# Performance work log

Hardware: AMD Instinct MI355X
Metric: run time of the kernel (lower is better)

The kernel has to match this reference:

```python
import jax, jax.numpy as jnp
import numpy as np

B, T, C, H, HS = 4, 2048, 1024, 16, 64
EPS = 1e-5


def setup_inputs() -> dict:
    key = jax.random.key(0)
    ks = jax.random.split(key, 16)
    s = lambda k, shp, fan: jax.random.normal(k, shp, jnp.float32) * (fan ** -0.5)
    return {
        "x": jax.random.normal(ks[0], (B, T, C), jnp.float32),
        "wq": s(ks[1], (H, C, HS), C), "bq": jnp.zeros((H, HS), jnp.float32),
        "wk": s(ks[2], (H, C, HS), C), "bk": jnp.zeros((H, HS), jnp.float32),
        "wv": s(ks[3], (H, C, HS), C), "bv": jnp.zeros((H, HS), jnp.float32),
        "wp": s(ks[4], (C, C), C), "bp": jnp.zeros((C,), jnp.float32),
        "w1": s(ks[5], (C, 4 * C), C), "b1": jnp.zeros((4 * C,), jnp.float32),
        "w2": s(ks[6], (4 * C, C), 4 * C), "b2": jnp.zeros((C,), jnp.float32),
        "g1": jnp.ones((C,), jnp.float32), "be1": jnp.zeros((C,), jnp.float32),
        "g2": jnp.ones((C,), jnp.float32), "be2": jnp.zeros((C,), jnp.float32),
    }


def _layernorm(x, g, b):
    mu = jnp.mean(x, axis=-1, keepdims=True)
    var = jnp.mean(jnp.square(x - mu), axis=-1, keepdims=True)
    return (x - mu) * jax.lax.rsqrt(var + EPS) * g + b


def reference(x, wq, bq, wk, bk, wv, bv, wp, bp, w1, b1, w2, b2, g1, be1, g2, be2):
    Bc, Tc, Cc = x.shape
    h = _layernorm(x, g1, be1)
    # per-head projections stacked: [B,H,T,HS]
    q = jnp.einsum('btc,hcd->bhtd', h, wq) + bq[None, :, None, :]
    k = jnp.einsum('btc,hcd->bhtd', h, wk) + bk[None, :, None, :]
    v = jnp.einsum('btc,hcd->bhtd', h, wv) + bv[None, :, None, :]
    # NOTE: source scales by 1/sqrt(n_embd), not 1/sqrt(head_size)
    scores = jnp.einsum('bhtd,bhsd->bhts', q, k) * (Cc ** -0.5)
    causal = jnp.tril(jnp.ones((Tc, Tc), bool))
    scores = jnp.where(causal, scores, -jnp.inf)
    attn = jax.nn.softmax(scores, axis=-1)
    out = jnp.einsum('bhts,bhsd->bhtd', attn, v)
    out = out.transpose(0, 2, 1, 3).reshape(Bc, Tc, Cc)  # concat heads
    x = x + out @ wp + bp
    h2 = _layernorm(x, g2, be2)
    ffn = jax.nn.relu(h2 @ w1 + b1) @ w2 + b2
    return x + ffn
```

## Files before the change

kernel.cpp:

```cpp
#include <hip/hip_runtime.h>


constexpr int Bb = 4, Tt = 2048, Cc = 1024, Hh = 16, HSz = 64, Ff = 4096;
constexpr int Mrows = Bb * Tt;

typedef __attribute__((ext_vector_type(8))) short bf16x8;
typedef __attribute__((ext_vector_type(4))) float f32x4;

__device__ __forceinline__ ushort f2bf(float f) {
  uint u = __builtin_bit_cast(uint, f);
  uint r = (u + 0x7fffu + ((u >> 16) & 1u)) >> 16;
  return (ushort)r;
}
__device__ __forceinline__ float bf2f(ushort s) {
  return __builtin_bit_cast(float, ((uint)s) << 16);
}
__device__ __forceinline__ uint cvtpk_bf16(float lo, float hi) {
  uint r;
  asm("v_cvt_pk_bf16_f32 %0, %1, %2" : "=v"(r) : "v"(lo), "v"(hi));
  return r;
}
__device__ __forceinline__ void gload16(const void* g, void* l) {
  __builtin_amdgcn_global_load_lds(
      (const __attribute__((address_space(1))) void*)g,
      (__attribute__((address_space(3))) void*)l, 16, 0, 0);
}
#define VMCNT0 asm volatile("s_waitcnt vmcnt(0)" ::: "memory")
#define LGKM0                                        \
  do {                                               \
    asm volatile("s_waitcnt lgkmcnt(0)" ::: "memory"); \
    __builtin_amdgcn_sched_barrier(0);               \
  } while (0)
#define BARRIER __builtin_amdgcn_s_barrier()

__global__ __launch_bounds__(256) void ln_kernel(const float* __restrict__ x,
                                                 const float* __restrict__ g,
                                                 const float* __restrict__ b,
                                                 ushort* __restrict__ out) {
  int row = blockIdx.x;
  const float* xr = x + (size_t)row * Cc;
  int c4 = threadIdx.x * 4;
  float4 v = *(const float4*)(xr + c4);
  float s1 = v.x + v.y + v.z + v.w;
  float s2 = v.x * v.x + v.y * v.y + v.z * v.z + v.w * v.w;
#pragma unroll
  for (int off = 32; off >= 1; off >>= 1) {
    s1 += __shfl_xor(s1, off);
    s2 += __shfl_xor(s2, off);
  }
  __shared__ float red[8];
  int wid = threadIdx.x >> 6, lane = threadIdx.x & 63;
  if (lane == 0) { red[wid] = s1; red[4 + wid] = s2; }
  __syncthreads();
  float t1 = red[0] + red[1] + red[2] + red[3];
  float t2 = red[4] + red[5] + red[6] + red[7];
  float mu = t1 * (1.0f / Cc);
  float var = t2 * (1.0f / Cc) - mu * mu;
  float rs = rsqrtf(var + 1e-5f);
  float4 gv = *(const float4*)(g + c4);
  float4 bv = *(const float4*)(b + c4);
  ushort4 o;
  o.x = f2bf((v.x - mu) * rs * gv.x + bv.x);
  o.y = f2bf((v.y - mu) * rs * gv.y + bv.y);
  o.z = f2bf((v.z - mu) * rs * gv.z + bv.z);
  o.w = f2bf((v.w - mu) * rs * gv.w + bv.w);
  *(ushort4*)(out + (size_t)row * Cc + c4) = o;
}

__device__ __forceinline__ void tcast_body(const float* __restrict__ src,
                                           ushort* __restrict__ dst, int ldS,
                                           int ldD, int r0, int c0) {
  __shared__ float t[32][33];
  int c = threadIdx.x & 31, r8 = threadIdx.x >> 5;
#pragma unroll
  for (int i = 0; i < 4; ++i) {
    int r = r8 + i * 8;
    t[r][c] = src[(size_t)(r0 + r) * ldS + c0 + c];
  }
  __syncthreads();
#pragma unroll
  for (int i = 0; i < 4; ++i) {
    int rr = r8 + i * 8;
    dst[(size_t)(c0 + rr) * ldD + r0 + c] = f2bf(t[c][rr]);
  }
}

__global__ __launch_bounds__(256) void tcast_kernel(const float* __restrict__ src,
                                                    ushort* __restrict__ dst,
                                                    int ldS, int ldD) {
  tcast_body(src, dst, ldS, ldD, blockIdx.x * 32, blockIdx.y * 32);
}

__global__ __launch_bounds__(256) void tcast_qkv(const float* __restrict__ wq,
                                                 const float* __restrict__ wk,
                                                 const float* __restrict__ wv,
                                                 ushort* __restrict__ dst) {
  int z = blockIdx.z, zz = z >> 4, h = z & 15;
  const float* src = (zz == 0 ? wq : (zz == 1 ? wk : wv)) + (size_t)h * Cc * HSz;
  ushort* d = dst + (size_t)(zz * 1024 + h * 64) * 1024;
  tcast_body(src, d, HSz, Cc, blockIdx.x * 32, blockIdx.y * 32);
}

__global__ __launch_bounds__(256) void bias_concat(const float* __restrict__ bq,
                                                   const float* __restrict__ bk,
                                                   const float* __restrict__ bv,
                                                   float* __restrict__ dst) {
  int i = blockIdx.x * 256 + threadIdx.x;
  dst[i] = i < 1024 ? bq[i] : (i < 2048 ? bk[i - 1024] : bv[i - 2048]);
}

__device__ __forceinline__ void xcd_swz(int& bx, int& by) {
  int bid = blockIdx.x + blockIdx.y * gridDim.x;
  int cpx = (gridDim.x * gridDim.y) >> 3;
  int id = (bid & 7) * cpx + (bid >> 3);
  bx = id % gridDim.x;
  by = id / gridDim.x;
}

template <int MH, int NH>
__device__ __forceinline__ void mfma16(f32x4 (&acc)[8][4], bf16x8 (&a)[4][2],
                                       bf16x8 (&b)[2][2]) {
#pragma unroll
  for (int m = 0; m < 4; ++m)
#pragma unroll
    for (int n = 0; n < 2; ++n)
#pragma unroll
      for (int kk = 0; kk < 2; ++kk)
        acc[MH * 4 + m][NH * 2 + n] = __builtin_amdgcn_mfma_f32_16x16x32_bf16(
            a[m][kk], b[n][kk], acc[MH * 4 + m][NH * 2 + n], 0, 0, 0);
}

__device__ __forceinline__ void gemm256_main(const ushort* __restrict__ A,
                                             const ushort* __restrict__ Bt,
                                             int m0, int n0,
                                             ushort* __restrict__ As,
                                             ushort* __restrict__ Bs,
                                             f32x4 (&acc)[8][4]) {
  constexpr int NKT = 16;
  int tid = threadIdx.x, wid = tid >> 6, lane = tid & 63;
  int wr = wid >> 2, wc = wid & 3, fr = lane & 15, fq = lane >> 4;
  const ushort* Ag = A + (size_t)m0 * 1024;
  const ushort* Bg = Bt + (size_t)n0 * 1024;
  int r0 = tid >> 3, r1 = 64 + (tid >> 3);
  int sc = ((tid & 7) ^ ((tid >> 3) & 7)) << 3;

  auto stage = [&](int ktn, int h, int ns) {
    const ushort* g = (h < 2) ? Ag : Bg;
    ushort* l = ((h < 2) ? As : Bs) + ns * 16384 + (h & 1) * 8192;
    int kcol = ktn * 64, rbase = (h & 1) * 128;
    gload16(g + (size_t)(rbase + r0) * 1024 + kcol + sc, l + (size_t)wid * 512);
    gload16(g + (size_t)(rbase + r1) * 1024 + kcol + sc,
            l + (size_t)(512 + wid * 64) * 8);
  };
  auto readA = [&](int slot, int mh, bf16x8 (&a)[4][2]) {
#pragma unroll
    for (int m = 0; m < 4; ++m) {
      int row = wr * 128 + mh * 64 + m * 16 + fr;
#pragma unroll
      for (int kk = 0; kk < 2; ++kk)
        a[m][kk] = *(const bf16x8*)&As[slot * 16384 + row * 64 +
                                       (((kk * 4 + fq) ^ (row & 7)) << 3)];
    }
  };
  auto readB = [&](int slot, int nh, bf16x8 (&b)[2][2]) {
#pragma unroll
    for (int n = 0; n < 2; ++n) {
      int row = wc * 64 + nh * 32 + n * 16 + fr;
#pragma unroll
      for (int kk = 0; kk < 2; ++kk)
        b[n][kk] = *(const bf16x8*)&Bs[slot * 16384 + row * 64 +
                                       (((kk * 4 + fq) ^ (row & 7)) << 3)];
    }
  };

  stage(0, 0, 0); stage(0, 1, 0); stage(0, 2, 0); stage(0, 3, 0);
  VMCNT0;
  BARRIER;

  bf16x8 a[4][2], b0[2][2], b1[2][2];
#pragma unroll 1
  for (int kt = 0; kt < NKT; ++kt) {
    int slot = kt & 1, ns = slot ^ 1;
    bool st = (kt + 1 < NKT);
    readA(slot, 0, a);
    readB(slot, 0, b0);
    if (st) { stage(kt + 1, 0, ns); stage(kt + 1, 2, ns); }
    BARRIER;
    LGKM0;
    __builtin_amdgcn_s_setprio(1);
    mfma16<0, 0>(acc, a, b0);
    __builtin_amdgcn_s_setprio(0);
    BARRIER;
    readB(slot, 1, b1);
    if (st) { stage(kt + 1, 1, ns); stage(kt + 1, 3, ns); }
    BARRIER;
    LGKM0;
    __builtin_amdgcn_s_setprio(1);
    mfma16<0, 1>(acc, a, b1);
    __builtin_amdgcn_s_setprio(0);
    BARRIER;
    readA(slot, 1, a);
    BARRIER;
    LGKM0;
    __builtin_amdgcn_s_setprio(1);
    mfma16<1, 0>(acc, a, b0);
    __builtin_amdgcn_s_setprio(0);
    BARRIER;
    __builtin_amdgcn_s_setprio(1);
    mfma16<1, 1>(acc, a, b1);
    __builtin_amdgcn_s_setprio(0);
    VMCNT0;
    BARRIER;
  }
}

__global__ __launch_bounds__(512, 2) void gemm256_relu(
    const ushort* __restrict__ A, const ushort* __restrict__ Bt,
    const float* __restrict__ bias, ushort* __restrict__ Cout, int ldc) {
  __shared__ __align__(16) ushort As[2 * 256 * 64];
  __shared__ __align__(16) ushort Bs[2 * 256 * 64];
  f32x4 acc[8][4] = {};
  int bx, by;
  xcd_swz(bx, by);
  int m0 = by * 256, n0 = bx * 256;
  gemm256_main(A, Bt, m0, n0, As, Bs, acc);
  int lane = threadIdx.x & 63, wid = threadIdx.x >> 6;
  int wr = wid >> 2, wc = wid & 3, fr = lane & 15, fq = lane >> 4;
#pragma unroll
  for (int i = 0; i < 8; ++i) {
    int gm = m0 + wr * 128 + (i >> 2) * 64 + (i & 3) * 16 + fq * 4;
#pragma unroll
    for (int j2 = 0; j2 < 4; ++j2) {
      int gn = n0 + wc * 64 + (j2 >> 1) * 32 + (j2 & 1) * 16 + fr;
      float bsv = bias[gn];
#pragma unroll
      for (int j = 0; j < 4; ++j)
        Cout[(size_t)(gm + j) * ldc + gn] = f2bf(fmaxf(acc[i][j2][j] + bsv, 0.f));
    }
  }
}

__global__ __launch_bounds__(512, 2) void gemm256_qkv(
    const ushort* __restrict__ A, const ushort* __restrict__ Bt,
    const float* __restrict__ bias, ushort* __restrict__ q,
    ushort* __restrict__ k, ushort* __restrict__ vt) {
  __shared__ __align__(16) ushort As[2 * 256 * 64];
  __shared__ __align__(16) ushort Bs[2 * 256 * 64];
  f32x4 acc[8][4] = {};
  int bx, by;
  xcd_swz(bx, by);
  int m0 = by * 256, n0 = bx * 256;
  gemm256_main(A, Bt, m0, n0, As, Bs, acc);
  int lane = threadIdx.x & 63, wid = threadIdx.x >> 6;
  int wr = wid >> 2, wc = wid & 3, fr = lane & 15, fq = lane >> 4;
  const float qscale = 1.4426950408889634f / 32.0f;
#pragma unroll
  for (int i = 0; i < 8; ++i) {
    int gm = m0 + wr * 128 + (i >> 2) * 64 + (i & 3) * 16 + fq * 4;
#pragma unroll
    for (int j2 = 0; j2 < 4; ++j2) {
      int gn = n0 + wc * 64 + (j2 >> 1) * 32 + (j2 & 1) * 16 + fr;
      float bsv = bias[gn];
      if (gn < 1024) {
#pragma unroll
        for (int j = 0; j < 4; ++j)
          q[(size_t)(gm + j) * 1024 + gn] = f2bf((acc[i][j2][j] + bsv) * qscale);
      } else if (gn < 2048) {
        int col = gn - 1024;
#pragma unroll
        for (int j = 0; j < 4; ++j)
          k[(size_t)(gm + j) * 1024 + col] = f2bf(acc[i][j2][j] + bsv);
      } else {
        int dd = gn - 2048, h = dd >> 6, d = dd & 63;
        int bbr = gm >> 11, t = gm & 2047;
        ushort4 pw = {f2bf(acc[i][j2][0] + bsv), f2bf(acc[i][j2][1] + bsv),
                      f2bf(acc[i][j2][2] + bsv), f2bf(acc[i][j2][3] + bsv)};
        *(ushort4*)&vt[(((size_t)(bbr * 16 + h)) * 64 + d) * 2048 + t] = pw;
      }
    }
  }
}

__device__ __forceinline__ void gemm_main(const ushort* __restrict__ A, int lda,
                                          const ushort* __restrict__ Bt, int ldb,
                                          int K, int m0, int n0,
                                          ushort* __restrict__ As,
                                          ushort* __restrict__ Bs,
                                          f32x4 (&acc)[4][2]) {
  int tid = threadIdx.x, wid = tid >> 6, lane = tid & 63;
  int wr = wid >> 2, wc = wid & 3, fr = lane & 15, fq = lane >> 4;
  const ushort* Ag = A + (size_t)m0 * lda;
  const ushort* Bg = Bt + (size_t)n0 * ldb;
  for (int k0 = 0; k0 < K; k0 += 64) {
#pragma unroll
    for (int c = 0; c < 2; ++c) {
      int slot = c * 512 + tid;
      int row = slot >> 3, s = slot & 7;
      int sw = (s << 3) ^ ((row & 7) << 3);
      gload16(Ag + (size_t)row * lda + k0 + sw, As + (size_t)(c * 512 + wid * 64) * 8);
      gload16(Bg + (size_t)row * ldb + k0 + sw, Bs + (size_t)(c * 512 + wid * 64) * 8);
    }
    __syncthreads();
    bf16x8 av[4][2], bv[2][2];
#pragma unroll
    for (int m = 0; m < 4; ++m) {
      int row = wr * 64 + m * 16 + fr;
#pragma unroll
      for (int ks = 0; ks < 2; ++ks)
        av[m][ks] = *(const bf16x8*)&As[row * 64 + (((ks * 4 + fq) ^ (row & 7)) << 3)];
    }
#pragma unroll
    for (int n = 0; n < 2; ++n) {
      int row = wc * 32 + n * 16 + fr;
#pragma unroll
      for (int ks = 0; ks < 2; ++ks)
        bv[n][ks] = *(const bf16x8*)&Bs[row * 64 + (((ks * 4 + fq) ^ (row & 7)) << 3)];
    }
#pragma unroll
    for (int m = 0; m < 4; ++m)
#pragma unroll
      for (int n = 0; n < 2; ++n)
#pragma unroll
        for (int ks = 0; ks < 2; ++ks)
          acc[m][n] = __builtin_amdgcn_mfma_f32_16x16x32_bf16(
              av[m][ks], bv[n][ks], acc[m][n], 0, 0, 0);
    __syncthreads();
  }
}

template <bool RELU, bool HASRES, bool OUTBF16>
__global__ __launch_bounds__(512) void gemm_bf16(
    const ushort* __restrict__ A, int lda, const ushort* __restrict__ Bt,
    int ldb, const float* __restrict__ bias, const float* __restrict__ res,
    void* __restrict__ Cout, int ldc, int K) {
  __shared__ __align__(16) ushort As[128 * 64];
  __shared__ __align__(16) ushort Bs[128 * 64];
  f32x4 acc[4][2] = {};
  int bx, by;
  xcd_swz(bx, by);
  int m0 = by * 128, n0 = bx * 128;
  gemm_main(A, lda, Bt, ldb, K, m0, n0, As, Bs, acc);
  int lane = threadIdx.x & 63, wid = threadIdx.x >> 6;
  int wr = wid >> 2, wc = wid & 3, fr = lane & 15, fq = lane >> 4;
#pragma unroll
  for (int m = 0; m < 4; ++m) {
    int gm = m0 + wr * 64 + m * 16 + fq * 4;
#pragma unroll
    for (int n = 0; n < 2; ++n) {
      int gn = n0 + wc * 32 + n * 16 + fr;
      float bsv = bias[gn];
#pragma unroll
      for (int j = 0; j < 4; ++j) {
        int row = gm + j;
        float v = acc[m][n][j] + bsv;
        if constexpr (HASRES) v += res[(size_t)row * ldc + gn];
        if constexpr (RELU) v = fmaxf(v, 0.f);
        if constexpr (OUTBF16)
          ((ushort*)Cout)[(size_t)row * ldc + gn] = f2bf(v);
        else
          ((float*)Cout)[(size_t)row * ldc + gn] = v;
      }
    }
  }
}

constexpr int QB = 128, KVB = 64;
__global__ __launch_bounds__(512) void attn_kernel(const ushort* __restrict__ Qb,
                                                   const ushort* __restrict__ Kb,
                                                   const ushort* __restrict__ Vt,
                                                   ushort* __restrict__ att) {
  __shared__ __align__(16) ushort Klds[2][64 * 64];
  __shared__ __align__(16) ushort Vlds[2][64 * 64];
  __shared__ __align__(16) ushort Plds[8][16 * 64];
  int tid = threadIdx.x, wid = tid >> 6, lane = tid & 63;
  int fr = lane & 15, fq = lane >> 4;
  int bh = blockIdx.y, bb = bh >> 4, hh = bh & 15;
  const ushort* qkbase = Qb + ((size_t)bb * Tt) * Cc + hh * HSz;
  const ushort* Kbase = Kb + ((size_t)bb * Tt) * Cc + hh * HSz;
  const ushort* Vbase = Vt + ((size_t)(bb * Hh + hh)) * HSz * Tt;
  int srow = tid >> 3;
  int ssw = ((tid & 7) << 3) ^ ((srow & 7) << 3);

#pragma unroll 1
  for (int pass = 0; pass < 2; ++pass) {
    int qt = pass ? (Tt / QB - 1 - (int)blockIdx.x) : (int)blockIdx.x;
    int q0 = qt * QB;
    int q0w = q0 + wid * 16;

    bf16x8 Qreg[2];
#pragma unroll
    for (int d2 = 0; d2 < 2; ++d2)
      Qreg[d2] = *(const bf16x8*)(qkbase + (size_t)(q0w + fr) * Cc + d2 * 32 + fq * 8);
    f32x4 Oa[4] = {};
    float mrow = -1e30f, lrow = 0.f;
    int nt = q0 / KVB + 2;

    __syncthreads();
    gload16(Kbase + (size_t)srow * Cc + ssw, (char*)Klds[0] + wid * 1024);
    gload16(Vbase + (size_t)srow * Tt + ssw, (char*)Vlds[0] + wid * 1024);

#pragma unroll 1
    for (int kt = 0; kt < nt; ++kt) {
      int t0 = kt * KVB;
      int c = kt & 1;
      __syncthreads();
      if (kt + 1 < nt) {
        int t0n = t0 + KVB;
        gload16(Kbase + (size_t)(t0n + srow) * Cc + ssw,
                (char*)Klds[c ^ 1] + wid * 1024);
        gload16(Vbase + (size_t)srow * Tt + t0n + ssw,
                (char*)Vlds[c ^ 1] + wid * 1024);
      }
      if (q0w + 15 < t0) continue;

      const char* Kc = (const char*)Klds[c];
      const char* Vc = (const char*)Vlds[c];
      bf16x8 kf[4][2];
#pragma unroll
      for (int ks = 0; ks < 4; ++ks)
#pragma unroll
        for (int d2 = 0; d2 < 2; ++d2) {
          int row = ks * 16 + fr;
          int off = (d2 * 64 + fq * 16) ^ ((row & 7) << 4);
          kf[ks][d2] = *(const bf16x8*)(Kc + row * 128 + off);
        }
      f32x4 accs[4] = {};
      __builtin_amdgcn_s_setprio(1);
#pragma unroll
      for (int ks = 0; ks < 4; ++ks) {
        accs[ks] = __builtin_amdgcn_mfma_f32_16x16x32_bf16(
            kf[ks][0], Qreg[0], accs[ks], 0, 0, 0);
        accs[ks] = __builtin_amdgcn_mfma_f32_16x16x32_bf16(
            kf[ks][1], Qreg[1], accs[ks], 0, 0, 0);
      }
      __builtin_amdgcn_s_setprio(0);

      float sv[4][4];
      float vmax = -1e30f;
      if (t0 + 63 <= q0w) {
#pragma unroll
        for (int ks = 0; ks < 4; ++ks)
#pragma unroll
          for (int j = 0; j < 4; ++j) {
            sv[ks][j] = accs[ks][j];
            vmax = fmaxf(vmax, sv[ks][j]);
          }
      } else {
        int qg = q0w + fr;
#pragma unroll
        for (int ks = 0; ks < 4; ++ks)
#pragma unroll
          for (int j = 0; j < 4; ++j) {
            int kg = t0 + ks * 16 + fq * 4 + j;
            float s = accs[ks][j];
            s = (kg <= qg) ? s : -1e30f;
            sv[ks][j] = s;
            vmax = fmaxf(vmax, s);
          }
      }
      float mnew = mrow;
      if (!__all(vmax <= mrow + 11.0f)) {
        float rmax = fmaxf(vmax, __shfl_xor(vmax, 16));
        rmax = fmaxf(rmax, __shfl_xor(rmax, 32));
        mnew = fmaxf(mrow, rmax);
        float sf = exp2f(mrow - mnew);
        mrow = mnew;
        lrow *= sf;
#pragma unroll
        for (int j = 0; j < 4; ++j) {
          float sfo = __shfl(sf, fq * 4 + j);
#pragma unroll
          for (int ds = 0; ds < 4; ++ds) Oa[ds][j] *= sfo;
        }
      }
      char* pbase = (char*)Plds[wid] + fr * 128;
#pragma unroll
      for (int ks = 0; ks < 4; ++ks) {
        float p0 = exp2f(sv[ks][0] - mnew);
        float p1 = exp2f(sv[ks][1] - mnew);
        float p2 = exp2f(sv[ks][2] - mnew);
        float p3 = exp2f(sv[ks][3] - mnew);
        lrow += (p0 + p1) + (p2 + p3);
        uint2 pw = {cvtpk_bf16(p0, p1), cvtpk_bf16(p2, p3)};
        int off = (ks * 32 + fq * 8) ^ ((fr & 7) << 4);
        *(uint2*)(pbase + off) = pw;
      }

      bf16x8 vf[4][2];
#pragma unroll
      for (int ds = 0; ds < 4; ++ds)
#pragma unroll
        for (int k2 = 0; k2 < 2; ++k2) {
          int row = ds * 16 + fr;
          int off = (k2 * 64 + fq * 16) ^ ((row & 7) << 4);
          vf[ds][k2] = *(const bf16x8*)(Vc + row * 128 + off);
        }
      bf16x8 pf[2];
#pragma unroll
      for (int k2 = 0; k2 < 2; ++k2) {
        int off = (k2 * 64 + fq * 16) ^ ((fr & 7) << 4);
        pf[k2] = *(const bf16x8*)((const char*)Plds[wid] + fr * 128 + off);
      }
      __builtin_amdgcn_s_setprio(1);
#pragma unroll
      for (int ds = 0; ds < 4; ++ds) {
        Oa[ds] = __builtin_amdgcn_mfma_f32_16x16x32_bf16(
            pf[0], vf[ds][0], Oa[ds], 0, 0, 0);
        Oa[ds] = __builtin_amdgcn_mfma_f32_16x16x32_bf16(
            pf[1], vf[ds][1], Oa[ds], 0, 0, 0);
      }
      __builtin_amdgcn_s_setprio(0);
    }

    {
      lrow += __shfl_xor(lrow, 16);
      lrow += __shfl_xor(lrow, 32);
      float linv = 1.f / lrow;
#pragma unroll
      for (int j = 0; j < 4; ++j) {
        float lo = __shfl(linv, fq * 4 + j);
        int qg = q0w + fq * 4 + j;
        ushort* orow = att + (size_t)(bb * Tt + qg) * Cc + hh * HSz;
#pragma unroll
        for (int ds = 0; ds < 4; ++ds)
          orow[ds * 16 + fr] = f2bf(Oa[ds][j] * lo);
      }
    }
  }
}

extern "C" void kernel_launch(void* const* d_in, const int* in_sizes, int n_in,
                              void* d_out, int out_size, void* d_ws,
                              size_t ws_size, hipStream_t stream) {
  const float* x = (const float*)d_in[0];
  const float* wq = (const float*)d_in[1];
  const float* bq = (const float*)d_in[2];
  const float* wk = (const float*)d_in[3];
  const float* bk = (const float*)d_in[4];
  const float* wv = (const float*)d_in[5];
  const float* bv = (const float*)d_in[6];
  const float* wp = (const float*)d_in[7];
  const float* bp = (const float*)d_in[8];
  const float* w1 = (const float*)d_in[9];
  const float* b1 = (const float*)d_in[10];
  const float* w2 = (const float*)d_in[11];
  const float* b2 = (const float*)d_in[12];
  const float* g1 = (const float*)d_in[13];
  const float* be1 = (const float*)d_in[14];
  const float* g2 = (const float*)d_in[15];
  const float* be2 = (const float*)d_in[16];
  float* out = (float*)d_out;

  ushort* Qb = (ushort*)d_ws;
  ushort* Kb = Qb + (size_t)8388608;
  ushort* Vt = Kb + (size_t)8388608;
  ushort* att = Vt + (size_t)8388608;
  ushort* ffh = Qb;
  ushort* h1b = att + (size_t)8388608;
  float* x2 = (float*)(h1b + (size_t)8388608);
  ushort* wqkvT = (ushort*)(x2 + (size_t)8388608);
  ushort* wpT = wqkvT + (size_t)3145728;
  ushort* w1T = wpT + (size_t)1048576;
  ushort* w2T = w1T + (size_t)4194304;
  float* bqkv = (float*)(w2T + (size_t)4194304);

  tcast_qkv<<<dim3(32, 2, 48), 256, 0, stream>>>(wq, wk, wv, wqkvT);
  tcast_kernel<<<dim3(32, 32), 256, 0, stream>>>(wp, wpT, 1024, 1024);
  tcast_kernel<<<dim3(32, 128), 256, 0, stream>>>(w1, w1T, 4096, 1024);
  tcast_kernel<<<dim3(128, 32), 256, 0, stream>>>(w2, w2T, 1024, 4096);
  bias_concat<<<dim3(12), 256, 0, stream>>>(bq, bk, bv, bqkv);

  ln_kernel<<<dim3(Mrows), 256, 0, stream>>>(x, g1, be1, h1b);
  gemm256_qkv<<<dim3(12, 32), 512, 0, stream>>>(h1b, wqkvT, bqkv, Qb, Kb, Vt);
  attn_kernel<<<dim3(Tt / QB / 2, Bb * Hh), 512, 0, stream>>>(Qb, Kb, Vt, att);
  gemm_bf16<false, true, false><<<dim3(8, 64), 512, 0, stream>>>(
      att, 1024, wpT, 1024, bp, x, x2, 1024, 1024);
  ln_kernel<<<dim3(Mrows), 256, 0, stream>>>(x2, g2, be2, h1b);
  gemm256_relu<<<dim3(16, 32), 512, 0, stream>>>(h1b, w1T, b1, ffh, 4096);
  gemm_bf16<false, true, false><<<dim3(8, 64), 512, 0, stream>>>(
      ffh, 4096, w2T, 4096, b2, x2, out, 1024, 4096);
}
```

Baseline: 358.2 us.

## Use 256x128 pipelined GEMM for FFN2 and 128x128 tiles for QKV

Adds a new 256x128-tile FFN down-projection kernel with double-buffered LDS staging, swizzled reads, split MFMA phases and raised wave priority. It replaces the 128x128 generic GEMM for the K=4096 projection and reuses more data per tile. In exchange, the QKV projection moves from the 256x256 kernel to the generic 128x128 kernel, which gives more blocks (1536 vs 384) for better occupancy and balance but less reuse per block. The new FFN2 grid has only 256 blocks, which may underfill the GPU.

```diff
diff --git a/kernel.cpp b/kernel.cpp
--- a/kernel.cpp
+++ b/kernel.cpp
@@ -26,10 +26,10 @@
       (__attribute__((address_space(3))) void*)l, 16, 0, 0);
 }
 #define VMCNT0 asm volatile("s_waitcnt vmcnt(0)" ::: "memory")
-#define LGKM0                                        \
-  do {                                               \
+#define LGKM0                                          \
+  do {                                                 \
     asm volatile("s_waitcnt lgkmcnt(0)" ::: "memory"); \
-    __builtin_amdgcn_sched_barrier(0);               \
+    __builtin_amdgcn_sched_barrier(0);                 \
   } while (0)
 #define BARRIER __builtin_amdgcn_s_barrier()
 
@@ -240,42 +240,114 @@
   }
 }
 
-__global__ __launch_bounds__(512, 2) void gemm256_qkv(
-    const ushort* __restrict__ A, const ushort* __restrict__ Bt,
-    const float* __restrict__ bias, ushort* __restrict__ q,
-    ushort* __restrict__ k, ushort* __restrict__ vt) {
+__global__ __launch_bounds__(512, 2) void gemm256_ffn2(
+    const ushort* __restrict__ A, int lda, const ushort* __restrict__ Bt,
+    int ldb, const float* __restrict__ bias, const float* __restrict__ res,
+    float* __restrict__ Cout, int ldc, int K) {
   __shared__ __align__(16) ushort As[2 * 256 * 64];
-  __shared__ __align__(16) ushort Bs[2 * 256 * 64];
-  f32x4 acc[8][4] = {};
+  __shared__ __align__(16) ushort Bs[2 * 128 * 64];
+  f32x4 acc[8][2] = {};
   int bx, by;
   xcd_swz(bx, by);
-  int m0 = by * 256, n0 = bx * 256;
-  gemm256_main(A, Bt, m0, n0, As, Bs, acc);
-  int lane = threadIdx.x & 63, wid = threadIdx.x >> 6;
+  int m0 = by * 256, n0 = bx * 128;
+  int tid = threadIdx.x, wid = tid >> 6, lane = tid & 63;
   int wr = wid >> 2, wc = wid & 3, fr = lane & 15, fq = lane >> 4;
-  const float qscale = 1.4426950408889634f / 32.0f;
+  const ushort* Ag = A + (size_t)m0 * lda;
+  const ushort* Bg = Bt + (size_t)n0 * ldb;
+  int r0 = tid >> 3, r1 = 64 + (tid >> 3);
+  int sc = ((tid & 7) ^ ((tid >> 3) & 7)) << 3;
+  int NKT = K >> 6;
+
+  auto stageA = [&](int ktn, int h, int ns) {
+    ushort* l = As + ns * 16384 + h * 8192;
+    int kcol = ktn * 64, rbase = h * 128;
+    gload16(Ag + (size_t)(rbase + r0) * lda + kcol + sc, l + (size_t)wid * 512);
+    gload16(Ag + (size_t)(rbase + r1) * lda + kcol + sc,
+            l + (size_t)(512 + wid * 64) * 8);
+  };
+  auto stageB = [&](int ktn, int h, int ns) {
+    ushort* l = Bs + ns * 8192 + h * 4096;
+    int kcol = ktn * 64, rbase = h * 64;
+    gload16(Bg + (size_t)(rbase + r0) * ldb + kcol + sc, l + (size_t)wid * 512);
+  };
+  auto readA = [&](int slot, int mh, bf16x8 (&a)[4][2]) {
+#pragma unroll
+    for (int m = 0; m < 4; ++m) {
+      int row = wr * 128 + mh * 64 + m * 16 + fr;
+#pragma unroll
+      for (int kk = 0; kk < 2; ++kk)
+        a[m][kk] = *(const bf16x8*)&As[slot * 16384 + row * 64 +
+                                       (((kk * 4 + fq) ^ (row & 7)) << 3)];
+    }
+  };
+  auto readB = [&](int slot, int nh, bf16x8 (&b)[2]) {
+    int row = wc * 32 + nh * 16 + fr;
+#pragma unroll
+    for (int kk = 0; kk < 2; ++kk)
+      b[kk] = *(const bf16x8*)&Bs[slot * 8192 + row * 64 +
+                                  (((kk * 4 + fq) ^ (row & 7)) << 3)];
+  };
+  auto mfma8 = [&](int mh, int nh, bf16x8 (&a)[4][2], bf16x8 (&b)[2]) {
+#pragma unroll
+    for (int m = 0; m < 4; ++m)
+#pragma unroll
+      for (int kk = 0; kk < 2; ++kk)
+        acc[mh * 4 + m][nh] = __builtin_amdgcn_mfma_f32_16x16x32_bf16(
+            a[m][kk], b[kk], acc[mh * 4 + m][nh], 0, 0, 0);
+  };
+
+  stageA(0, 0, 0); stageA(0, 1, 0); stageB(0, 0, 0); stageB(0, 1, 0);
+  VMCNT0;
+  BARRIER;
+
+  bf16x8 a[4][2], b0[2], b1[2];
+#pragma unroll 1
+  for (int kt = 0; kt < NKT; ++kt) {
+    int slot = kt & 1, ns = slot ^ 1;
+    bool st = (kt + 1 < NKT);
+    readA(slot, 0, a);
+    readB(slot, 0, b0);
+    if (st) { stageA(kt + 1, 0, ns); stageB(kt + 1, 0, ns); }
+    BARRIER;
+    LGKM0;
+    __builtin_amdgcn_s_setprio(1);
+    mfma8(0, 0, a, b0);
+    __builtin_amdgcn_s_setprio(0);
+    BARRIER;
+    readB(slot, 1, b1);
+    if (st) { stageA(kt + 1, 1, ns); stageB(kt + 1, 1, ns); }
+    BARRIER;
+    LGKM0;
+    __builtin_amdgcn_s_setprio(1);
+    mfma8(0, 1, a, b1);
+    __builtin_amdgcn_s_setprio(0);
+    BARRIER;
+    readA(slot, 1, a);
+    BARRIER;
+    LGKM0;
+    __builtin_amdgcn_s_setprio(1);
+    mfma8(1, 0, a, b0);
+    __builtin_amdgcn_s_setprio(0);
+    BARRIER;
+    __builtin_amdgcn_s_setprio(1);
+    mfma8(1, 1, a, b1);
+    __builtin_amdgcn_s_setprio(0);
+    VMCNT0;
+    BARRIER;
+  }
+
 #pragma unroll
   for (int i = 0; i < 8; ++i) {
     int gm = m0 + wr * 128 + (i >> 2) * 64 + (i & 3) * 16 + fq * 4;
 #pragma unroll
-    for (int j2 = 0; j2 < 4; ++j2) {
-      int gn = n0 + wc * 64 + (j2 >> 1) * 32 + (j2 & 1) * 16 + fr;
+    for (int nh = 0; nh < 2; ++nh) {
+      int gn = n0 + wc * 32 + nh * 16 + fr;
       float bsv = bias[gn];
-      if (gn < 1024) {
-#pragma unroll
-        for (int j = 0; j < 4; ++j)
-          q[(size_t)(gm + j) * 1024 + gn] = f2bf((acc[i][j2][j] + bsv) * qscale);
-      } else if (gn < 2048) {
-        int col = gn - 1024;
-#pragma unroll
-        for (int j = 0; j < 4; ++j)
-          k[(size_t)(gm + j) * 1024 + col] = f2bf(acc[i][j2][j] + bsv);
-      } else {
-        int dd = gn - 2048, h = dd >> 6, d = dd & 63;
-        int bbr = gm >> 11, t = gm & 2047;
-        ushort4 pw = {f2bf(acc[i][j2][0] + bsv), f2bf(acc[i][j2][1] + bsv),
-                      f2bf(acc[i][j2][2] + bsv), f2bf(acc[i][j2][3] + bsv)};
-        *(ushort4*)&vt[(((size_t)(bbr * 16 + h)) * 64 + d) * 2048 + t] = pw;
+#pragma unroll
+      for (int j = 0; j < 4; ++j) {
+        int row = gm + j;
+        Cout[(size_t)row * ldc + gn] =
+            acc[i][nh][j] + bsv + res[(size_t)row * ldc + gn];
       }
     }
   }
@@ -359,6 +431,49 @@
           ((ushort*)Cout)[(size_t)row * ldc + gn] = f2bf(v);
         else
           ((float*)Cout)[(size_t)row * ldc + gn] = v;
+      }
+    }
+  }
+}
+
+__global__ __launch_bounds__(512) void gemm_qkv(const ushort* __restrict__ A,
+                                                const ushort* __restrict__ Bt,
+                                                const float* __restrict__ bias,
+                                                ushort* __restrict__ q,
+                                                ushort* __restrict__ k,
+                                                ushort* __restrict__ vt) {
+  __shared__ __align__(16) ushort As[128 * 64];
+  __shared__ __align__(16) ushort Bs[128 * 64];
+  f32x4 acc[4][2] = {};
+  int bx, by;
+  xcd_swz(bx, by);
+  int m0 = by * 128, n0 = bx * 128;
+  gemm_main(A, 1024, Bt, 1024, 1024, m0, n0, As, Bs, acc);
+  int lane = threadIdx.x & 63, wid = threadIdx.x >> 6;
+  int wr = wid >> 2, wc = wid & 3, fr = lane & 15, fq = lane >> 4;
+  const float qscale = 1.4426950408889634f / 32.0f;
+#pragma unroll
+  for (int m = 0; m < 4; ++m) {
+    int gm = m0 + wr * 64 + m * 16 + fq * 4;
+#pragma unroll
+    for (int n = 0; n < 2; ++n) {
+      int gn = n0 + wc * 32 + n * 16 + fr;
+      float bsv = bias[gn];
+      if (gn < 1024) {
+#pragma unroll
+        for (int j = 0; j < 4; ++j)
+          q[(size_t)(gm + j) * 1024 + gn] = f2bf((acc[m][n][j] + bsv) * qscale);
+      } else if (gn < 2048) {
+        int col = gn - 1024;
+#pragma unroll
+        for (int j = 0; j < 4; ++j)
+          k[(size_t)(gm + j) * 1024 + col] = f2bf(acc[m][n][j] + bsv);
+      } else {
+        int dd = gn - 2048, h = dd >> 6, d = dd & 63;
+        int bbr = gm >> 11, t = gm & 2047;
+        ushort4 pw = {f2bf(acc[m][n][0] + bsv), f2bf(acc[m][n][1] + bsv),
+                      f2bf(acc[m][n][2] + bsv), f2bf(acc[m][n][3] + bsv)};
+        *(ushort4*)&vt[(((size_t)(bbr * 16 + h)) * 64 + d) * 2048 + t] = pw;
       }
     }
   }
@@ -571,12 +686,12 @@
   bias_concat<<<dim3(12), 256, 0, stream>>>(bq, bk, bv, bqkv);
 
   ln_kernel<<<dim3(Mrows), 256, 0, stream>>>(x, g1, be1, h1b);
-  gemm256_qkv<<<dim3(12, 32), 512, 0, stream>>>(h1b, wqkvT, bqkv, Qb, Kb, Vt);
+  gemm_qkv<<<dim3(24, 64), 512, 0, stream>>>(h1b, wqkvT, bqkv, Qb, Kb, Vt);
   attn_kernel<<<dim3(Tt / QB / 2, Bb * Hh), 512, 0, stream>>>(Qb, Kb, Vt, att);
   gemm_bf16<false, true, false><<<dim3(8, 64), 512, 0, stream>>>(
       att, 1024, wpT, 1024, bp, x, x2, 1024, 1024);
   ln_kernel<<<dim3(Mrows), 256, 0, stream>>>(x2, g2, be2, h1b);
   gemm256_relu<<<dim3(16, 32), 512, 0, stream>>>(h1b, w1T, b1, ffh, 4096);
-  gemm_bf16<false, true, false><<<dim3(8, 64), 512, 0, stream>>>(
+  gemm256_ffn2<<<dim3(8, 32), 512, 0, stream>>>(
       ffh, 4096, w2T, 4096, b2, x2, out, 1024, 4096);
 }
```

New measurement: 364.8 us. No clear change (+1.8%).
